# Kernel optimization log

Measured on AMD Instinct MI355X. Metric: run time of the kernel, lower is better.

The kernel has to match this reference:

```python
import jax, jax.numpy as jnp
import numpy as np
from jax import lax

B, C, H, W = 16, 64, 160, 160
K, O, KS = 8, 64, 3
A = 16  # attention_channel = max(int(64*0.0625), 16)
EPS = 1e-5


def setup_inputs() -> dict:
    key = jax.random.key(0)
    ks = jax.random.split(key, 16)
    return {
        'x': jax.random.normal(ks[0], (B, C, H, W), jnp.float32),
        'scale': jnp.ones((2,), jnp.float32) * 2.0,  # (scale_h, scale_w)
        'rw1': jax.random.normal(ks[1], (2 * C, C + 2), jnp.float32) * 0.1,
        'rb1': jnp.zeros((2 * C,), jnp.float32),
        'rw2': jax.random.normal(ks[2], (C, 2 * C), jnp.float32) * 0.1,
        'rb2': jnp.zeros((C,), jnp.float32),
        'fc_w': jax.random.normal(ks[3], (A, C), jnp.float32) * 0.1,
        'bn_gamma': jnp.ones((A,), jnp.float32),
        'bn_beta': jnp.zeros((A,), jnp.float32),
        'bn_mean': jax.random.normal(ks[4], (A,), jnp.float32) * 0.1,
        'bn_var': jax.random.uniform(ks[5], (A,), jnp.float32, 0.5, 1.5),
        'cfc_w': jax.random.normal(ks[6], (C, A), jnp.float32) * 0.1,
        'cfc_b': jnp.zeros((C,), jnp.float32),
        'ffc_w': jax.random.normal(ks[7], (O, A), jnp.float32) * 0.1,
        'ffc_b': jnp.zeros((O,), jnp.float32),
        'sfc_w': jax.random.normal(ks[8], (KS * KS, A), jnp.float32) * 0.1,
        'sfc_b': jnp.zeros((KS * KS,), jnp.float32),
        'kfc_w': jax.random.normal(ks[9], (K, A), jnp.float32) * 0.1,
        'kfc_b': jnp.zeros((K,), jnp.float32),
        'weight': jax.random.normal(ks[10], (K, O, C, KS, KS), jnp.float32) * 0.05,
    }


def reference(x, scale, rw1, rb1, rw2, rb2, fc_w, bn_gamma, bn_beta, bn_mean,
              bn_var, cfc_w, cfc_b, ffc_w, ffc_b, sfc_w, sfc_b, kfc_w, kfc_b,
              weight):
    b, c, h, w = x.shape
    k_num, o, cg, ks, _ = weight.shape
    # scale routing MLP: concat [1/sh, 1/sw, GAP(x)] -> relu(Linear) -> relu(Linear)
    gap = x.mean(axis=(2, 3))  # [B, C]
    scale_info = jnp.broadcast_to(1.0 / scale, (b, 2))
    s = jnp.concatenate([scale_info, gap], axis=1)  # [B, C+2]
    s = jax.nn.relu(s @ rw1.T + rb1)
    routed = jax.nn.relu(s @ rw2.T + rb2)  # [B, C]
    # ScaleAttention trunk: 1x1 conv (no bias) + BN(eval) + ReLU on [B,C,1,1]
    v = routed @ fc_w.T  # [B, A]
    v = (v - bn_mean) * lax.rsqrt(bn_var + EPS) * bn_gamma + bn_beta
    v = jax.nn.relu(v)
    # four attention heads (temperature = 1.0)
    channel_att = jax.nn.sigmoid(v @ cfc_w.T + cfc_b)            # [B, C]
    filter_att = jax.nn.sigmoid(v @ ffc_w.T + ffc_b)             # [B, O]
    spatial_att = jax.nn.sigmoid(v @ sfc_w.T + sfc_b).reshape(b, 1, 1, 1, ks, ks)
    kernel_att = jax.nn.softmax(v @ kfc_w.T + kfc_b, axis=1).reshape(b, k_num, 1, 1, 1, 1)
    # channel-gate input, aggregate per-sample dynamic kernels over experts
    xc = x * channel_att[:, :, None, None]
    agg_w = jnp.sum(spatial_att * kernel_att * weight[None], axis=1)  # [B,O,C,ks,ks]
    agg_w = agg_w.reshape(b * o, cg, ks, ks)
    # grouped-conv trick: groups = batch (original groups=1)
    out = lax.conv_general_dilated(
        xc.reshape(1, b * c, h, w), agg_w,
        window_strides=(1, 1), padding=((1, 1), (1, 1)),
        feature_group_count=b,
        dimension_numbers=('NCHW', 'OIHW', 'NCHW'))
    out = out.reshape(b, o, h, w) * filter_att[:, :, None, None]
    return out
```

## Files before the change

kernel.cpp:

```cpp
#include <hip/hip_runtime.h>
#include <math.h>

#define BB 16
#define CC 64
#define HH 160
#define WW 160
#define KK 8
#define OO 64
#define AA 16
#define HWQ (HH * WW)

typedef __attribute__((ext_vector_type(8))) short sh8;
typedef __attribute__((ext_vector_type(4))) float fx4;

__device__ inline unsigned short f2bf(float f) {
    unsigned int u = __float_as_uint(f);
    return (unsigned short)((u + 0x7FFFu + ((u >> 16) & 1u)) >> 16);
}
__device__ inline float bf2f(unsigned short h) {
    return __uint_as_float(((unsigned int)h) << 16);
}

__global__ __launch_bounds__(256) void trans_kernel(
    const float* __restrict__ x,
    unsigned short* __restrict__ xt_hi, unsigned short* __restrict__ xt_lo,
    float* __restrict__ pg) {
    __shared__ float ts[64][84];
    const int half = blockIdx.x;
    const int h    = blockIdx.y;
    const int b    = blockIdx.z;
    const int w0   = half * 80;
    const int tid  = threadIdx.x;

    for (int i = tid; i < 1280; i += 256) {
        int c  = i / 20;
        int wq = i % 20;
        float4 v = *(const float4*)(
            x + (((size_t)(b * CC + c)) * HH + h) * WW + w0 + wq * 4);
        *(float4*)(&ts[c][wq * 4]) = v;
    }
    __syncthreads();

    if (tid < 64) {
        float s = 0.f;
        #pragma unroll 10
        for (int w = 0; w < 80; ++w) s += ts[tid][w];
        pg[((size_t)b * 320 + h * 2 + half) * 64 + tid] = s;
    }

    for (int i = tid; i < 640; i += 256) {
        int g = i & 7;
        int w = i >> 3;
        sh8 vh, vl;
        #pragma unroll
        for (int e = 0; e < 8; ++e) {
            float v = ts[g * 8 + e][w];
            unsigned short hh = f2bf(v);
            vh[e] = (short)hh;
            vl[e] = (short)f2bf(v - bf2f(hh));
        }
        size_t off = (((size_t)(b * HH + h)) * WW + w0 + w) * CC + g * 8;
        *(sh8*)(xt_hi + off) = vh;
        *(sh8*)(xt_lo + off) = vl;
    }
}

__global__ __launch_bounds__(128) void mlp_kernel(
    const float* __restrict__ scale,
    const float* __restrict__ rw1, const float* __restrict__ rb1,
    const float* __restrict__ rw2, const float* __restrict__ rb2,
    const float* __restrict__ fc_w,
    const float* __restrict__ bn_gamma, const float* __restrict__ bn_beta,
    const float* __restrict__ bn_mean, const float* __restrict__ bn_var,
    const float* __restrict__ cfc_w, const float* __restrict__ cfc_b,
    const float* __restrict__ ffc_w, const float* __restrict__ ffc_b,
    const float* __restrict__ sfc_w, const float* __restrict__ sfc_b,
    const float* __restrict__ kfc_w, const float* __restrict__ kfc_b,
    const float* __restrict__ pg,
    float* __restrict__ ca, float* __restrict__ fa,
    float* __restrict__ sa, float* __restrict__ ka) {
    int b = blockIdx.x;
    int t = threadIdx.x;
    __shared__ float sin_[CC + 2];
    __shared__ float h1[2 * CC];
    __shared__ float h2[CC];
    __shared__ float vv[AA];
    __shared__ float kl[KK];

    if (t < 2) sin_[t] = 1.0f / scale[t];
    if (t < CC) {
        float s = 0.f;
        for (int h2v = 0; h2v < 320; ++h2v)
            s += pg[((size_t)b * 320 + h2v) * 64 + t];
        sin_[2 + t] = s * (1.0f / (float)HWQ);
    }
    __syncthreads();

    {
        float a = rb1[t];
        const float* wr = rw1 + (size_t)t * (CC + 2);
        #pragma unroll 6
        for (int j = 0; j < CC + 2; ++j) a += sin_[j] * wr[j];
        h1[t] = fmaxf(a, 0.f);
    }
    __syncthreads();

    if (t < CC) {
        float a = rb2[t];
        const float* wr = rw2 + (size_t)t * (2 * CC);
        #pragma unroll 8
        for (int j = 0; j < 2 * CC; ++j) a += h1[j] * wr[j];
        h2[t] = fmaxf(a, 0.f);
    }
    __syncthreads();

    if (t < AA) {
        float a = 0.f;
        const float* wr = fc_w + (size_t)t * CC;
        #pragma unroll 8
        for (int j = 0; j < CC; ++j) a += h2[j] * wr[j];
        a = (a - bn_mean[t]) * rsqrtf(bn_var[t] + 1e-5f) * bn_gamma[t] + bn_beta[t];
        vv[t] = fmaxf(a, 0.f);
    }
    __syncthreads();

    if (t < CC) {
        float a = cfc_b[t];
        const float* wr = cfc_w + (size_t)t * AA;
        #pragma unroll
        for (int j = 0; j < AA; ++j) a += vv[j] * wr[j];
        ca[b * CC + t] = 1.f / (1.f + expf(-a));
        float f = ffc_b[t];
        const float* wf = ffc_w + (size_t)t * AA;
        #pragma unroll
        for (int j = 0; j < AA; ++j) f += vv[j] * wf[j];
        fa[b * CC + t] = 1.f / (1.f + expf(-f));
    }
    if (t < 9) {
        float a = sfc_b[t];
        const float* wr = sfc_w + (size_t)t * AA;
        #pragma unroll
        for (int j = 0; j < AA; ++j) a += vv[j] * wr[j];
        sa[b * 16 + t] = 1.f / (1.f + expf(-a));
    }
    if (t < KK) {
        float a = kfc_b[t];
        const float* wr = kfc_w + (size_t)t * AA;
        #pragma unroll
        for (int j = 0; j < AA; ++j) a += vv[j] * wr[j];
        kl[t] = a;
    }
    __syncthreads();
    if (t < KK) {
        float m = kl[0];
        #pragma unroll
        for (int j = 1; j < KK; ++j) m = fmaxf(m, kl[j]);
        float sum = 0.f;
        #pragma unroll
        for (int j = 0; j < KK; ++j) sum += expf(kl[j] - m);
        ka[b * KK + t] = expf(kl[t] - m) / sum;
    }
}

__global__ __launch_bounds__(256) void agg_frag_kernel(
    const float* __restrict__ weight,
    const float* __restrict__ ca, const float* __restrict__ fa,
    const float* __restrict__ sa, const float* __restrict__ ka,
    unsigned short* __restrict__ Ahi, unsigned short* __restrict__ Alo) {
    int e = blockIdx.x * 256 + threadIdx.x;
    int q  = e % 9;
    int t2 = e / 9;
    int c  = t2 & 63;
    int bo = t2 >> 6;
    int o  = bo & 63;
    int b  = bo >> 6;
    float s = 0.f;
    #pragma unroll
    for (int k = 0; k < KK; ++k)
        s += ka[b * KK + k] * weight[(((size_t)(k * OO + o)) * CC + c) * 9 + q];
    float val = s * sa[b * 16 + q] * ca[b * CC + c] * fa[b * CC + o];
    unsigned short hi = f2bf(val);
    unsigned short lo = f2bf(val - bf2f(hi));
    int mt = o >> 4;
    int lane = (o & 15) | (((c >> 3) & 3) << 4);
    int j = c & 7;
    int ch = c >> 5;
    size_t off = ((((size_t)(b * 9 + q) * 2 + ch) * 4 + mt) * 64 + lane) * 8 + j;
    Ahi[off] = hi;
    Alo[off] = lo;
}

__global__ __launch_bounds__(256) void conv_mfma_kernel(
    const unsigned short* __restrict__ xt_hi,
    const unsigned short* __restrict__ xt_lo,
    const unsigned short* __restrict__ Ahi,
    const unsigned short* __restrict__ Alo,
    float* __restrict__ out) {
    __shared__ __align__(16) unsigned short xs_hi[10 * 18 * 64];
    __shared__ __align__(16) unsigned short xs_lo[10 * 18 * 64];

    const int b  = blockIdx.z;
    const int h0 = blockIdx.y * 8;
    const int w0 = blockIdx.x * 16;
    const int tid  = threadIdx.x;
    const int wv   = tid >> 6;
    const int lane = tid & 63;

    for (int i = tid; i < 10 * 18 * 8; i += 256) {
        int g   = i & 7;
        int col = (i >> 3) % 18;
        int row = i / 144;
        int gh = h0 - 1 + row;
        int gw = w0 - 1 + col;
        uint4 vhi = {0u, 0u, 0u, 0u}, vlo = {0u, 0u, 0u, 0u};
        if ((unsigned)gh < (unsigned)HH && (unsigned)gw < (unsigned)WW) {
            size_t off = (((size_t)(b * HH + gh)) * WW + gw) * CC + g * 8;
            vhi = *(const uint4*)(xt_hi + off);
            vlo = *(const uint4*)(xt_lo + off);
        }
        int lidx = (row * 18 + col) * 64 + ((g ^ (col & 7)) << 3);
        *(uint4*)(&xs_hi[lidx]) = vhi;
        *(uint4*)(&xs_lo[lidx]) = vlo;
    }
    __syncthreads();

    fx4 z = {0.f, 0.f, 0.f, 0.f};
    fx4 acc[2][4] = {{z, z, z, z}, {z, z, z, z}};

    const int lr = lane & 15;
    const int l4 = lane >> 4;

    #pragma unroll
    for (int q = 0; q < 9; ++q) {
        const int kh = q / 3, kw = q % 3;
        const int col = lr + kw;
        #pragma unroll
        for (int ch = 0; ch < 2; ++ch) {
            const int g  = ch * 4 + l4;
            const int cg = (g ^ (col & 7)) << 3;
            sh8 bhi[2], blo[2];
            #pragma unroll
            for (int nr = 0; nr < 2; ++nr) {
                const int row  = wv * 2 + nr + kh;
                const int lidx = (row * 18 + col) * 64 + cg;
                bhi[nr] = *(const sh8*)(&xs_hi[lidx]);
                blo[nr] = *(const sh8*)(&xs_lo[lidx]);
            }
            const size_t abase =
                ((size_t)((b * 9 + q) * 2 + ch)) * 2048 + lane * 8;
            #pragma unroll
            for (int mt = 0; mt < 4; ++mt) {
                sh8 a_hi = *(const sh8*)(Ahi + abase + mt * 512);
                sh8 a_lo = *(const sh8*)(Alo + abase + mt * 512);
                #pragma unroll
                for (int nr = 0; nr < 2; ++nr) {
                    acc[nr][mt] = __builtin_amdgcn_mfma_f32_16x16x32_bf16(
                        a_hi, bhi[nr], acc[nr][mt], 0, 0, 0);
                    acc[nr][mt] = __builtin_amdgcn_mfma_f32_16x16x32_bf16(
                        a_hi, blo[nr], acc[nr][mt], 0, 0, 0);
                    acc[nr][mt] = __builtin_amdgcn_mfma_f32_16x16x32_bf16(
                        a_lo, bhi[nr], acc[nr][mt], 0, 0, 0);
                }
            }
        }
    }

    #pragma unroll
    for (int nr = 0; nr < 2; ++nr) {
        const int hrow = h0 + wv * 2 + nr;
        #pragma unroll
        for (int mt = 0; mt < 4; ++mt) {
            #pragma unroll
            for (int jj = 0; jj < 4; ++jj) {
                int o = mt * 16 + l4 * 4 + jj;
                out[((size_t)(b * OO + o)) * HWQ + hrow * WW + w0 + lr] =
                    acc[nr][mt][jj];
            }
        }
    }
}

extern "C" void kernel_launch(void* const* d_in, const int* in_sizes, int n_in,
                              void* d_out, int out_size, void* d_ws, size_t ws_size,
                              hipStream_t stream) {
    const float* x        = (const float*)d_in[0];
    const float* scale    = (const float*)d_in[1];
    const float* rw1      = (const float*)d_in[2];
    const float* rb1      = (const float*)d_in[3];
    const float* rw2      = (const float*)d_in[4];
    const float* rb2      = (const float*)d_in[5];
    const float* fc_w     = (const float*)d_in[6];
    const float* bn_gamma = (const float*)d_in[7];
    const float* bn_beta  = (const float*)d_in[8];
    const float* bn_mean  = (const float*)d_in[9];
    const float* bn_var   = (const float*)d_in[10];
    const float* cfc_w    = (const float*)d_in[11];
    const float* cfc_b    = (const float*)d_in[12];
    const float* ffc_w    = (const float*)d_in[13];
    const float* ffc_b    = (const float*)d_in[14];
    const float* sfc_w    = (const float*)d_in[15];
    const float* sfc_b    = (const float*)d_in[16];
    const float* kfc_w    = (const float*)d_in[17];
    const float* kfc_b    = (const float*)d_in[18];
    const float* weight   = (const float*)d_in[19];

    const size_t WS_NEEDED = 107233280u;
    if (ws_size < WS_NEEDED) return;

    char* wsb = (char*)d_ws;
    float* ca  = (float*)(wsb + 0);
    float* fa  = (float*)(wsb + 4096);
    float* sa  = (float*)(wsb + 8192);
    float* ka  = (float*)(wsb + 12288);
    float* pg  = (float*)(wsb + 16384);
    unsigned short* Ahi  = (unsigned short*)(wsb + 16384);
    unsigned short* Alo  = (unsigned short*)(wsb + 1196032);
    unsigned short* xthi = (unsigned short*)(wsb + 2375680);
    unsigned short* xtlo = (unsigned short*)(wsb + 54804480);

    trans_kernel<<<dim3(2, 160, 16), dim3(256), 0, stream>>>(
        x, xthi, xtlo, pg);
    mlp_kernel<<<dim3(BB), dim3(128), 0, stream>>>(
        scale, rw1, rb1, rw2, rb2, fc_w, bn_gamma, bn_beta, bn_mean, bn_var,
        cfc_w, cfc_b, ffc_w, ffc_b, sfc_w, sfc_b, kfc_w, kfc_b,
        pg, ca, fa, sa, ka);
    agg_frag_kernel<<<dim3(589824 / 256), dim3(256), 0, stream>>>(
        weight, ca, fa, sa, ka, Ahi, Alo);
    conv_mfma_kernel<<<dim3(10, 20, 16), dim3(256), 0, stream>>>(
        xthi, xtlo, Ahi, Alo, (float*)d_out);
}
```

Baseline: 340.3 us.

## Software-pipeline MFMA operand loads in conv and pad transpose LDS rows

The conv inner loop becomes a flattened 18-step loop that prefetches the next step's A fragments from global memory and B fragments from LDS while the current step's MFMAs run. The MFMAs are reordered so consecutive instructions hit independent accumulators, avoiding back-to-back dependency stalls. Launch bounds request 3 blocks per SM. The transpose kernel's shared tile gets extra padding every 8 rows to cut bank conflicts, and the pg reduction loop is unrolled. The cost is higher register pressure, which the occupancy hint may force into spills.

```diff
diff --git a/kernel.cpp b/kernel.cpp
--- a/kernel.cpp
+++ b/kernel.cpp
@@ -21,11 +21,12 @@
     return __uint_as_float(((unsigned int)h) << 16);
 }
 
+#define TSROW(c) ((c) * 84 + (((c) >> 3) << 2))
 __global__ __launch_bounds__(256) void trans_kernel(
     const float* __restrict__ x,
     unsigned short* __restrict__ xt_hi, unsigned short* __restrict__ xt_lo,
     float* __restrict__ pg) {
-    __shared__ float ts[64][84];
+    __shared__ float ts[5408];
     const int half = blockIdx.x;
     const int h    = blockIdx.y;
     const int b    = blockIdx.z;
@@ -37,14 +38,15 @@
         int wq = i % 20;
         float4 v = *(const float4*)(
             x + (((size_t)(b * CC + c)) * HH + h) * WW + w0 + wq * 4);
-        *(float4*)(&ts[c][wq * 4]) = v;
+        *(float4*)(&ts[TSROW(c) + wq * 4]) = v;
     }
     __syncthreads();
 
     if (tid < 64) {
         float s = 0.f;
+        const float* row = &ts[TSROW(tid)];
         #pragma unroll 10
-        for (int w = 0; w < 80; ++w) s += ts[tid][w];
+        for (int w = 0; w < 80; ++w) s += row[w];
         pg[((size_t)b * 320 + h * 2 + half) * 64 + tid] = s;
     }
 
@@ -54,7 +56,7 @@
         sh8 vh, vl;
         #pragma unroll
         for (int e = 0; e < 8; ++e) {
-            float v = ts[g * 8 + e][w];
+            float v = ts[TSROW(g * 8 + e) + w];
             unsigned short hh = f2bf(v);
             vh[e] = (short)hh;
             vl[e] = (short)f2bf(v - bf2f(hh));
@@ -90,6 +92,7 @@
     if (t < 2) sin_[t] = 1.0f / scale[t];
     if (t < CC) {
         float s = 0.f;
+        #pragma unroll 8
         for (int h2v = 0; h2v < 320; ++h2v)
             s += pg[((size_t)b * 320 + h2v) * 64 + t];
         sin_[2 + t] = s * (1.0f / (float)HWQ);
@@ -190,7 +193,7 @@
     Alo[off] = lo;
 }
 
-__global__ __launch_bounds__(256) void conv_mfma_kernel(
+__global__ __launch_bounds__(256, 3) void conv_mfma_kernel(
     const unsigned short* __restrict__ xt_hi,
     const unsigned short* __restrict__ xt_lo,
     const unsigned short* __restrict__ Ahi,
@@ -230,38 +233,70 @@
     const int lr = lane & 15;
     const int l4 = lane >> 4;
 
-    #pragma unroll
-    for (int q = 0; q < 9; ++q) {
-        const int kh = q / 3, kw = q % 3;
-        const int col = lr + kw;
-        #pragma unroll
-        for (int ch = 0; ch < 2; ++ch) {
-            const int g  = ch * 4 + l4;
-            const int cg = (g ^ (col & 7)) << 3;
-            sh8 bhi[2], blo[2];
+    const unsigned short* Ah = Ahi + (size_t)b * 36864 + lane * 8;
+    const unsigned short* Al = Alo + (size_t)b * 36864 + lane * 8;
+
+    auto bofs = [&](int s, int nr) -> int {
+        int q = s >> 1, ch = s & 1;
+        int kh = q / 3, kw = q % 3;
+        int col = lr + kw;
+        int row = wv * 2 + nr + kh;
+        int g = ch * 4 + l4;
+        return (row * 18 + col) * 64 + ((g ^ (col & 7)) << 3);
+    };
+
+    sh8 cah[4], cal[4], cbh[2], cbl[2];
+    #pragma unroll
+    for (int mt = 0; mt < 4; ++mt) {
+        cah[mt] = *(const sh8*)(Ah + mt * 512);
+        cal[mt] = *(const sh8*)(Al + mt * 512);
+    }
+    #pragma unroll
+    for (int nr = 0; nr < 2; ++nr) {
+        int li = bofs(0, nr);
+        cbh[nr] = *(const sh8*)(&xs_hi[li]);
+        cbl[nr] = *(const sh8*)(&xs_lo[li]);
+    }
+
+    #pragma unroll
+    for (int s = 0; s < 18; ++s) {
+        sh8 nah[4], nal[4], nbh[2], nbl[2];
+        if (s < 17) {
+            #pragma unroll
+            for (int mt = 0; mt < 4; ++mt) {
+                nah[mt] = *(const sh8*)(Ah + (s + 1) * 2048 + mt * 512);
+                nal[mt] = *(const sh8*)(Al + (s + 1) * 2048 + mt * 512);
+            }
             #pragma unroll
             for (int nr = 0; nr < 2; ++nr) {
-                const int row  = wv * 2 + nr + kh;
-                const int lidx = (row * 18 + col) * 64 + cg;
-                bhi[nr] = *(const sh8*)(&xs_hi[lidx]);
-                blo[nr] = *(const sh8*)(&xs_lo[lidx]);
+                int li = bofs(s + 1, nr);
+                nbh[nr] = *(const sh8*)(&xs_hi[li]);
+                nbl[nr] = *(const sh8*)(&xs_lo[li]);
             }
-            const size_t abase =
-                ((size_t)((b * 9 + q) * 2 + ch)) * 2048 + lane * 8;
-            #pragma unroll
-            for (int mt = 0; mt < 4; ++mt) {
-                sh8 a_hi = *(const sh8*)(Ahi + abase + mt * 512);
-                sh8 a_lo = *(const sh8*)(Alo + abase + mt * 512);
-                #pragma unroll
-                for (int nr = 0; nr < 2; ++nr) {
-                    acc[nr][mt] = __builtin_amdgcn_mfma_f32_16x16x32_bf16(
-                        a_hi, bhi[nr], acc[nr][mt], 0, 0, 0);
-                    acc[nr][mt] = __builtin_amdgcn_mfma_f32_16x16x32_bf16(
-                        a_hi, blo[nr], acc[nr][mt], 0, 0, 0);
-                    acc[nr][mt] = __builtin_amdgcn_mfma_f32_16x16x32_bf16(
-                        a_lo, bhi[nr], acc[nr][mt], 0, 0, 0);
-                }
-            }
+        }
+        #pragma unroll
+        for (int nr = 0; nr < 2; ++nr)
+            #pragma unroll
+            for (int mt = 0; mt < 4; ++mt)
+                acc[nr][mt] = __builtin_amdgcn_mfma_f32_16x16x32_bf16(
+                    cah[mt], cbh[nr], acc[nr][mt], 0, 0, 0);
+        #pragma unroll
+        for (int nr = 0; nr < 2; ++nr)
+            #pragma unroll
+            for (int mt = 0; mt < 4; ++mt)
+                acc[nr][mt] = __builtin_amdgcn_mfma_f32_16x16x32_bf16(
+                    cah[mt], cbl[nr], acc[nr][mt], 0, 0, 0);
+        #pragma unroll
+        for (int nr = 0; nr < 2; ++nr)
+            #pragma unroll
+            for (int mt = 0; mt < 4; ++mt)
+                acc[nr][mt] = __builtin_amdgcn_mfma_f32_16x16x32_bf16(
+                    cal[mt], cbh[nr], acc[nr][mt], 0, 0, 0);
+        if (s < 17) {
+            #pragma unroll
+            for (int mt = 0; mt < 4; ++mt) { cah[mt] = nah[mt]; cal[mt] = nal[mt]; }
+            #pragma unroll
+            for (int nr = 0; nr < 2; ++nr) { cbh[nr] = nbh[nr]; cbl[nr] = nbl[nr]; }
         }
     }
 
```

After: 345.4 us. About the same (+1.5%).

## Double-buffer conv input tiles by channel half and process two row tiles per block

Applied to the files above, without the earlier changes.

The conv kernel now stages input in 32-channel halves into double-buffered shared memory. It issues global loads for the next stage into registers before computing the current stage. Each block handles two 8-row tiles (the grid is halved), and the launch bound now requests 3 blocks per CU. The A fragment layout is reordered so each channel half is contiguous, the transpose kernel pads its shared rows to avoid bank conflicts, and the GAP reduction loop is unrolled. The aim is to hide global load latency behind MFMA work, at the cost of more registers and fewer blocks.

```diff
diff --git a/kernel.cpp b/kernel.cpp
--- a/kernel.cpp
+++ b/kernel.cpp
@@ -21,11 +21,12 @@
     return __uint_as_float(((unsigned int)h) << 16);
 }
 
+#define TSROW(c) ((c) * 84 + (((c) >> 3) << 2))
 __global__ __launch_bounds__(256) void trans_kernel(
     const float* __restrict__ x,
     unsigned short* __restrict__ xt_hi, unsigned short* __restrict__ xt_lo,
     float* __restrict__ pg) {
-    __shared__ float ts[64][84];
+    __shared__ float ts[5408];
     const int half = blockIdx.x;
     const int h    = blockIdx.y;
     const int b    = blockIdx.z;
@@ -37,14 +38,15 @@
         int wq = i % 20;
         float4 v = *(const float4*)(
             x + (((size_t)(b * CC + c)) * HH + h) * WW + w0 + wq * 4);
-        *(float4*)(&ts[c][wq * 4]) = v;
+        *(float4*)(&ts[TSROW(c) + wq * 4]) = v;
     }
     __syncthreads();
 
     if (tid < 64) {
         float s = 0.f;
+        const float* row = &ts[TSROW(tid)];
         #pragma unroll 10
-        for (int w = 0; w < 80; ++w) s += ts[tid][w];
+        for (int w = 0; w < 80; ++w) s += row[w];
         pg[((size_t)b * 320 + h * 2 + half) * 64 + tid] = s;
     }
 
@@ -54,7 +56,7 @@
         sh8 vh, vl;
         #pragma unroll
         for (int e = 0; e < 8; ++e) {
-            float v = ts[g * 8 + e][w];
+            float v = ts[TSROW(g * 8 + e) + w];
             unsigned short hh = f2bf(v);
             vh[e] = (short)hh;
             vl[e] = (short)f2bf(v - bf2f(hh));
@@ -90,6 +92,7 @@
     if (t < 2) sin_[t] = 1.0f / scale[t];
     if (t < CC) {
         float s = 0.f;
+        #pragma unroll 8
         for (int h2v = 0; h2v < 320; ++h2v)
             s += pg[((size_t)b * 320 + h2v) * 64 + t];
         sin_[2 + t] = s * (1.0f / (float)HWQ);
@@ -185,99 +188,147 @@
     int lane = (o & 15) | (((c >> 3) & 3) << 4);
     int j = c & 7;
     int ch = c >> 5;
-    size_t off = ((((size_t)(b * 9 + q) * 2 + ch) * 4 + mt) * 64 + lane) * 8 + j;
+    size_t off = (((((size_t)b * 2 + ch) * 9 + q) * 4 + mt) * 64 + lane) * 8 + j;
     Ahi[off] = hi;
     Alo[off] = lo;
 }
 
-__global__ __launch_bounds__(256) void conv_mfma_kernel(
+__global__ __launch_bounds__(256, 3) void conv_mfma_kernel(
     const unsigned short* __restrict__ xt_hi,
     const unsigned short* __restrict__ xt_lo,
     const unsigned short* __restrict__ Ahi,
     const unsigned short* __restrict__ Alo,
     float* __restrict__ out) {
-    __shared__ __align__(16) unsigned short xs_hi[10 * 18 * 64];
-    __shared__ __align__(16) unsigned short xs_lo[10 * 18 * 64];
-
-    const int b  = blockIdx.z;
-    const int h0 = blockIdx.y * 8;
-    const int w0 = blockIdx.x * 16;
+    __shared__ __align__(16) unsigned short xs[2][2][720 * 8];
+
+    const int b   = blockIdx.z;
+    const int w0  = blockIdx.x * 16;
+    const int by2 = blockIdx.y * 2;
     const int tid  = threadIdx.x;
     const int wv   = tid >> 6;
     const int lane = tid & 63;
-
-    for (int i = tid; i < 10 * 18 * 8; i += 256) {
-        int g   = i & 7;
-        int col = (i >> 3) % 18;
-        int row = i / 144;
-        int gh = h0 - 1 + row;
-        int gw = w0 - 1 + col;
-        uint4 vhi = {0u, 0u, 0u, 0u}, vlo = {0u, 0u, 0u, 0u};
-        if ((unsigned)gh < (unsigned)HH && (unsigned)gw < (unsigned)WW) {
-            size_t off = (((size_t)(b * HH + gh)) * WW + gw) * CC + g * 8;
-            vhi = *(const uint4*)(xt_hi + off);
-            vlo = *(const uint4*)(xt_lo + off);
-        }
-        int lidx = (row * 18 + col) * 64 + ((g ^ (col & 7)) << 3);
-        *(uint4*)(&xs_hi[lidx]) = vhi;
-        *(uint4*)(&xs_lo[lidx]) = vlo;
-    }
-    __syncthreads();
+    const int lr = lane & 15;
+    const int l4 = lane >> 4;
+
+    const unsigned short* Ah = Ahi + (size_t)b * 36864 + lane * 8;
+    const unsigned short* Al = Alo + (size_t)b * 36864 + lane * 8;
+
+    uint4 sgh[3], sgl[3];
+
+    auto issue = [&](int t, int ch) {
+        const int h0t = (by2 + t) * 8;
+        #pragma unroll
+        for (int it = 0; it < 3; ++it) {
+            int j = it * 256 + tid;
+            int r = j / 72;
+            int rem = j - r * 72;
+            int c = rem >> 2, s = rem & 3;
+            int g = s ^ (c & 3);
+            int gh = h0t - 1 + r, gw = w0 - 1 + c;
+            uint4 vh = {0u, 0u, 0u, 0u}, vl = {0u, 0u, 0u, 0u};
+            if (j < 720 && (unsigned)gh < (unsigned)HH && (unsigned)gw < (unsigned)WW) {
+                size_t off = (((size_t)(b * HH + gh)) * WW + gw) * CC + ch * 32 + g * 8;
+                vh = *(const uint4*)(xt_hi + off);
+                vl = *(const uint4*)(xt_lo + off);
+            }
+            sgh[it] = vh;
+            sgl[it] = vl;
+        }
+    };
+
+    auto commit = [&](int bi) {
+        #pragma unroll
+        for (int it = 0; it < 3; ++it) {
+            int j = it * 256 + tid;
+            if (j < 720) {
+                *(uint4*)(&xs[bi][0][j * 8]) = sgh[it];
+                *(uint4*)(&xs[bi][1][j * 8]) = sgl[it];
+            }
+        }
+    };
 
     fx4 z = {0.f, 0.f, 0.f, 0.f};
     fx4 acc[2][4] = {{z, z, z, z}, {z, z, z, z}};
 
-    const int lr = lane & 15;
-    const int l4 = lane >> 4;
-
-    #pragma unroll
-    for (int q = 0; q < 9; ++q) {
-        const int kh = q / 3, kw = q % 3;
-        const int col = lr + kw;
-        #pragma unroll
-        for (int ch = 0; ch < 2; ++ch) {
-            const int g  = ch * 4 + l4;
-            const int cg = (g ^ (col & 7)) << 3;
-            sh8 bhi[2], blo[2];
+    auto compute = [&](int bi, int ch) {
+        #pragma unroll
+        for (int q = 0; q < 9; ++q) {
+            const int kh = q / 3, kw = q % 3;
+            const unsigned short* aph = Ah + (ch * 9 + q) * 2048;
+            const unsigned short* apl = Al + (ch * 9 + q) * 2048;
+            sh8 bh[2], bl[2];
+            const int col = lr + kw;
+            const int slot = l4 ^ (col & 3);
             #pragma unroll
             for (int nr = 0; nr < 2; ++nr) {
-                const int row  = wv * 2 + nr + kh;
-                const int lidx = (row * 18 + col) * 64 + cg;
-                bhi[nr] = *(const sh8*)(&xs_hi[lidx]);
-                blo[nr] = *(const sh8*)(&xs_lo[lidx]);
-            }
-            const size_t abase =
-                ((size_t)((b * 9 + q) * 2 + ch)) * 2048 + lane * 8;
+                int row = wv * 2 + nr + kh;
+                int j = row * 72 + col * 4 + slot;
+                bh[nr] = *(const sh8*)(&xs[bi][0][j * 8]);
+                bl[nr] = *(const sh8*)(&xs[bi][1][j * 8]);
+            }
             #pragma unroll
             for (int mt = 0; mt < 4; ++mt) {
-                sh8 a_hi = *(const sh8*)(Ahi + abase + mt * 512);
-                sh8 a_lo = *(const sh8*)(Alo + abase + mt * 512);
+                sh8 ah_ = *(const sh8*)(aph + mt * 512);
+                sh8 al_ = *(const sh8*)(apl + mt * 512);
                 #pragma unroll
                 for (int nr = 0; nr < 2; ++nr) {
                     acc[nr][mt] = __builtin_amdgcn_mfma_f32_16x16x32_bf16(
-                        a_hi, bhi[nr], acc[nr][mt], 0, 0, 0);
+                        ah_, bh[nr], acc[nr][mt], 0, 0, 0);
                     acc[nr][mt] = __builtin_amdgcn_mfma_f32_16x16x32_bf16(
-                        a_hi, blo[nr], acc[nr][mt], 0, 0, 0);
+                        ah_, bl[nr], acc[nr][mt], 0, 0, 0);
                     acc[nr][mt] = __builtin_amdgcn_mfma_f32_16x16x32_bf16(
-                        a_lo, bhi[nr], acc[nr][mt], 0, 0, 0);
+                        al_, bh[nr], acc[nr][mt], 0, 0, 0);
                 }
             }
         }
-    }
-
+    };
+
+    auto epilogue = [&](int t) {
+        const int h0t = (by2 + t) * 8;
+        #pragma unroll
+        for (int nr = 0; nr < 2; ++nr) {
+            const int hrow = h0t + wv * 2 + nr;
+            #pragma unroll
+            for (int mt = 0; mt < 4; ++mt) {
+                #pragma unroll
+                for (int jj = 0; jj < 4; ++jj) {
+                    int o = mt * 16 + l4 * 4 + jj;
+                    out[((size_t)(b * OO + o)) * HWQ + hrow * WW + w0 + lr] =
+                        acc[nr][mt][jj];
+                }
+            }
+        }
+    };
+
+    issue(0, 0);
+    commit(0);
+    __syncthreads();
+
+    issue(0, 1);
+    __builtin_amdgcn_sched_barrier(0);
+    compute(0, 0);
+    commit(1);
+    __syncthreads();
+
+    issue(1, 0);
+    __builtin_amdgcn_sched_barrier(0);
+    compute(1, 1);
+    commit(0);
+    epilogue(0);
     #pragma unroll
-    for (int nr = 0; nr < 2; ++nr) {
-        const int hrow = h0 + wv * 2 + nr;
-        #pragma unroll
-        for (int mt = 0; mt < 4; ++mt) {
-            #pragma unroll
-            for (int jj = 0; jj < 4; ++jj) {
-                int o = mt * 16 + l4 * 4 + jj;
-                out[((size_t)(b * OO + o)) * HWQ + hrow * WW + w0 + lr] =
-                    acc[nr][mt][jj];
-            }
-        }
-    }
+    for (int nr = 0; nr < 2; ++nr)
+        #pragma unroll
+        for (int mt = 0; mt < 4; ++mt) acc[nr][mt] = z;
+    __syncthreads();
+
+    issue(1, 1);
+    __builtin_amdgcn_sched_barrier(0);
+    compute(0, 0);
+    commit(1);
+    __syncthreads();
+
+    compute(1, 1);
+    epilogue(1);
 }
 
 extern "C" void kernel_launch(void* const* d_in, const int* in_sizes, int n_in,
@@ -326,6 +377,6 @@
         pg, ca, fa, sa, ka);
     agg_frag_kernel<<<dim3(589824 / 256), dim3(256), 0, stream>>>(
         weight, ca, fa, sa, ka, Ahi, Alo);
-    conv_mfma_kernel<<<dim3(10, 20, 16), dim3(256), 0, stream>>>(
+    conv_mfma_kernel<<<dim3(10, 10, 16), dim3(256), 0, stream>>>(
         xthi, xtlo, Ahi, Alo, (float*)d_out);
 }
```

New measurement: 483.2 us. 42.0% more time.
